# Optimization experiments

Measured on AMD Instinct MI355X. Metric: run time of the kernel, lower is better.

## Reference

```python
import jax, jax.numpy as jnp
import numpy as np

N = 50000      # nodes
E = 800000     # edges (avg degree 16)
IN = 128       # in_dim == hidden_dim*num_heads so residuals fire
D = 32         # hidden_dim (per-head)
H = 4          # num_heads
OUT = 64       # out_dim (final layer has 1 head)
NEG_SLOPE = 0.2
LN_EPS = 1e-5


def setup_inputs() -> dict:
    key = jax.random.key(0)
    ks = jax.random.split(key, 16)
    rn = lambda k, s: jax.random.normal(k, s, jnp.float32) * 0.05
    return {
        "features": jax.random.normal(ks[0], (N, IN), jnp.float32),
        "edge_weight": jax.random.uniform(ks[1], (E,), jnp.float32),
        "src": jax.random.randint(ks[2], (E,), 0, N),
        "dst": jax.random.randint(ks[3], (E,), 0, N),
        "W0": rn(ks[4], (IN, H * D)), "al0": rn(ks[5], (H, D)), "ar0": rn(ks[6], (H, D)), "lam0": jnp.float32(1.0),
        "W1": rn(ks[7], (H * D, H * D)), "al1": rn(ks[8], (H, D)), "ar1": rn(ks[9], (H, D)), "lam1": jnp.float32(1.0),
        "W2": rn(ks[10], (H * D, OUT)), "al2": rn(ks[11], (1, OUT)), "ar2": rn(ks[12], (1, OUT)), "lam2": jnp.float32(1.0),
        "g0": jnp.ones((H * D,), jnp.float32), "b0": jnp.zeros((H * D,), jnp.float32),
        "g1": jnp.ones((H * D,), jnp.float32), "b1": jnp.zeros((H * D,), jnp.float32),
    }


def _gat_layer(h, W, al, ar, lam, src, dst, ew):
    n = h.shape[0]
    heads, d = al.shape
    ft = (h @ W).reshape(n, heads, d)                      # [N,H,D]
    el = jnp.sum(ft * al[None], axis=-1)                   # [N,H]
    er = jnp.sum(ft * ar[None], axis=-1)                   # [N,H]
    e = el[src] + er[dst] + lam * ew[:, None]              # [E,H] u_add_v + weight bias
    e = jax.nn.leaky_relu(e, NEG_SLOPE)
    # edge softmax over incoming edges of each dst node
    m = jax.ops.segment_max(e, dst, num_segments=n)        # [N,H]
    ex = jnp.exp(e - m[dst])
    s = jax.ops.segment_sum(ex, dst, num_segments=n)       # [N,H]
    a = ex / s[dst]                                        # [E,H]
    # u_mul_e + sum aggregation
    msg = ft[src] * a[:, :, None]                          # [E,H,D]
    return jax.ops.segment_sum(msg, dst, num_segments=n)   # [N,H,D]


def _layer_norm(x, g, b):
    mu = jnp.mean(x, axis=-1, keepdims=True)
    var = jnp.mean((x - mu) ** 2, axis=-1, keepdims=True)
    return (x - mu) * jax.lax.rsqrt(var + LN_EPS) * g + b


def _forward(features, edge_weight, src, dst,
             W0, al0, ar0, lam0, W1, al1, ar1, lam1, W2, al2, ar2, lam2,
             g0, b0, g1, b1):
    n = features.shape[0]
    h = features
    # layer 0
    h1 = _gat_layer(h, W0, al0, ar0, lam0, src, dst, edge_weight)
    h1 = jax.nn.elu(h1).reshape(n, -1)
    h1 = _layer_norm(h1, g0, b0)
    if h1.shape == h.shape:
        h1 = h1 + h
    # layer 1
    h2 = _gat_layer(h1, W1, al1, ar1, lam1, src, dst, edge_weight)
    h2 = jax.nn.elu(h2).reshape(n, -1)
    h2 = _layer_norm(h2, g1, b1)
    h2 = h2 + h1
    # layer 2 (single head, no activation)
    out = _gat_layer(h2, W2, al2, ar2, lam2, src, dst, edge_weight).reshape(n, -1)
    return out


def reference(features, edge_weight, src, dst,
              W0, al0, ar0, lam0, W1, al1, ar1, lam1, W2, al2, ar2, lam2,
              g0, b0, g1, b1):
    # eval mode: dropout off and _add_noise is identity, so noisy == clean
    h_clean = _forward(features, edge_weight, src, dst,
                       W0, al0, ar0, lam0, W1, al1, ar1, lam1, W2, al2, ar2, lam2,
                       g0, b0, g1, b1)
    return (h_clean, h_clean)
```

## Files before the change

### kernel.cpp

```cpp
#include <hip/hip_runtime.h>

#define NEG_SLOPE 0.2f
#define LN_EPS 1e-5f

typedef __attribute__((ext_vector_type(8))) short bf16x8;
typedef __attribute__((ext_vector_type(4))) float f32x4;

__device__ inline unsigned short f2bf(float f) {
    unsigned u = __float_as_uint(f);
    unsigned r = u + 0x7FFFu + ((u >> 16) & 1u);
    return (unsigned short)(r >> 16);
}


__global__ void rank_kernel(const int* __restrict__ dst, int* __restrict__ counts,
                            int* __restrict__ rank, int E) {
    int i = blockIdx.x * blockDim.x + threadIdx.x;
    if (i < E) rank[i] = atomicAdd(&counts[dst[i] * 16], 1);
}

__global__ __launch_bounds__(256) void scan1_kernel(const int* __restrict__ counts,
                                                    int* __restrict__ bsum, int n) {
    __shared__ int lds[256];
    int t = threadIdx.x;
    int i = blockIdx.x * 256 + t;
    lds[t] = (i < n) ? counts[i * 16] : 0;
    __syncthreads();
    for (int off = 128; off > 0; off >>= 1) {
        int v = (t < off) ? lds[t + off] : 0;
        __syncthreads();
        if (t < off) lds[t] += v;
        __syncthreads();
    }
    if (t == 0) bsum[blockIdx.x] = lds[0];
}

__global__ __launch_bounds__(256) void scan2_kernel(int* __restrict__ bsum, int nblocks) {
    __shared__ int lds[256];
    int t = threadIdx.x;
    int v0 = (t < nblocks) ? bsum[t] : 0;
    lds[t] = v0;
    __syncthreads();
    for (int off = 1; off < 256; off <<= 1) {
        int v = (t >= off) ? lds[t - off] : 0;
        __syncthreads();
        lds[t] += v;
        __syncthreads();
    }
    if (t < nblocks) bsum[t] = lds[t] - v0;
}

__global__ __launch_bounds__(256) void scan3_kernel(const int* __restrict__ counts,
                                                    const int* __restrict__ bsum,
                                                    int* __restrict__ rowptr, int n, int E) {
    __shared__ int lds[256];
    int t = threadIdx.x;
    int i = blockIdx.x * 256 + t;
    int c = (i < n) ? counts[i * 16] : 0;
    lds[t] = c;
    __syncthreads();
    for (int off = 1; off < 256; off <<= 1) {
        int v = (t >= off) ? lds[t - off] : 0;
        __syncthreads();
        lds[t] += v;
        __syncthreads();
    }
    if (i < n) rowptr[i] = bsum[blockIdx.x] + lds[t] - c;
    if (i == n) rowptr[n] = E;
}

__global__ void place_kernel(const int* __restrict__ src, const int* __restrict__ dst,
                             const float* __restrict__ ew, const int* __restrict__ rowptr,
                             const int* __restrict__ rank, unsigned* __restrict__ edge_p,
                             int E) {
    int i = blockIdx.x * blockDim.x + threadIdx.x;
    if (i < E) {
        int p = rowptr[dst[i]] + rank[i];
        edge_p[p] = ((unsigned)f2bf(ew[i]) << 16) | (unsigned)src[i];
    }
}


__global__ void wcast_kernel(const float* __restrict__ W, unsigned short* __restrict__ Wt,
                             int ncols) {
    int n = blockIdx.x;
    int k = threadIdx.x;
    Wt[n * 128 + k] = f2bf(W[k * ncols + n]);
}


template <int NT, int H>
__global__ __launch_bounds__(256) void gemm_mfma(const float* __restrict__ A,
                                                 const unsigned short* __restrict__ Wt,
                                                 const float* __restrict__ al,
                                                 const float* __restrict__ ar,
                                                 unsigned short* __restrict__ ftb,
                                                 float* __restrict__ el,
                                                 float* __restrict__ er, int n) {
    constexpr int LDA = 136;
    constexpr int D = NT * 16 / H;
    __shared__ unsigned short As[64 * LDA];
    __shared__ unsigned short Ws[NT * 16 * LDA];
    int t = threadIdx.x;
    int row0 = blockIdx.x * 64;

    const float4* A4 = (const float4*)A;
    #pragma unroll
    for (int j = 0; j < 8; ++j) {
        int idx = t + j * 256;
        int r = idx >> 5;
        int c4 = idx & 31;
        int row = row0 + r;
        float4 v = (row < n) ? A4[(size_t)row * 32 + c4] : make_float4(0.f, 0.f, 0.f, 0.f);
        unsigned p0 = (unsigned)f2bf(v.x) | ((unsigned)f2bf(v.y) << 16);
        unsigned p1 = (unsigned)f2bf(v.z) | ((unsigned)f2bf(v.w) << 16);
        *(uint2*)&As[r * LDA + c4 * 4] = make_uint2(p0, p1);
    }
    const uint4* Wg = (const uint4*)Wt;
    #pragma unroll
    for (int j = 0; j < NT; ++j) {
        int idx = t + j * 256;
        int r = idx >> 4;
        int c8 = idx & 15;
        *(uint4*)&Ws[r * LDA + c8 * 8] = Wg[idx];
    }
    __syncthreads();

    int w = t >> 6, lane = t & 63;
    int m = lane & 15, q = lane >> 4;
    f32x4 acc[NT] = {};
    const unsigned short* ap = &As[(w * 16 + m) * LDA + q * 8];
    #pragma unroll
    for (int kk = 0; kk < 4; ++kk) {
        bf16x8 a = *(const bf16x8*)(ap + kk * 32);
        #pragma unroll
        for (int nt = 0; nt < NT; ++nt) {
            bf16x8 b = *(const bf16x8*)&Ws[(nt * 16 + m) * LDA + kk * 32 + q * 8];
            acc[nt] = __builtin_amdgcn_mfma_f32_16x16x32_bf16(a, b, acc[nt], 0, 0, 0);
        }
    }

    float alv[NT], arv[NT];
    #pragma unroll
    for (int nt = 0; nt < NT; ++nt) {
        alv[nt] = al[nt * 16 + m];
        arv[nt] = ar[nt * 16 + m];
    }

    int orow = row0 + w * 16 + q * 4;
    #pragma unroll
    for (int r = 0; r < 4; ++r) {
        int row = orow + r;
        float pl[H] = {}, pr[H] = {};
        #pragma unroll
        for (int nt = 0; nt < NT; ++nt) {
            int h = (nt * 16) / D;
            pl[h] = fmaf(acc[nt][r], alv[nt], pl[h]);
            pr[h] = fmaf(acc[nt][r], arv[nt], pr[h]);
        }
        #pragma unroll
        for (int off = 1; off < 16; off <<= 1) {
            #pragma unroll
            for (int h = 0; h < H; ++h) {
                pl[h] += __shfl_xor(pl[h], off, 64);
                pr[h] += __shfl_xor(pr[h], off, 64);
            }
        }
        if (row < n) {
            #pragma unroll
            for (int nt = 0; nt < NT; ++nt)
                ftb[(size_t)row * (NT * 16) + nt * 16 + m] = f2bf(acc[nt][r]);
            if (m < H) {
                float vl = pl[0], vr = pr[0];
                #pragma unroll
                for (int h = 1; h < H; ++h)
                    if (m == h) { vl = pl[h]; vr = pr[h]; }
                el[row * H + m] = vl;
                er[row * H + m] = vr;
            }
        }
    }
}


__device__ inline void accum8(float* ax, uint4 u, float p) {
    ax[0] = fmaf(p, __uint_as_float(u.x << 16), ax[0]);
    ax[1] = fmaf(p, __uint_as_float(u.x & 0xFFFF0000u), ax[1]);
    ax[2] = fmaf(p, __uint_as_float(u.y << 16), ax[2]);
    ax[3] = fmaf(p, __uint_as_float(u.y & 0xFFFF0000u), ax[3]);
    ax[4] = fmaf(p, __uint_as_float(u.z << 16), ax[4]);
    ax[5] = fmaf(p, __uint_as_float(u.z & 0xFFFF0000u), ax[5]);
    ax[6] = fmaf(p, __uint_as_float(u.w << 16), ax[6]);
    ax[7] = fmaf(p, __uint_as_float(u.w & 0xFFFF0000u), ax[7]);
}

__global__ __launch_bounds__(256) void gat_agg_ln(
    const int* __restrict__ rowptr, const unsigned* __restrict__ edge_p,
    const uint4* __restrict__ ftb4, const float* __restrict__ el,
    const float* __restrict__ er, const float* __restrict__ lam_p,
    const float* __restrict__ g, const float* __restrict__ b,
    const float* __restrict__ prev, float* __restrict__ out, int n) {
    int node = blockIdx.x * 16 + (threadIdx.x >> 4);
    if (node >= n) return;
    int li = threadIdx.x & 15;
    int head = li >> 2;
    float lam = lam_p[0];
    float erv = er[node * 4 + head];
    int s0 = rowptr[node], s1 = rowptr[node + 1];
    float ax[8] = {};
    float s = 0.f;

    int i = s0;
    for (; i + 2 <= s1; i += 2) {
        unsigned e0 = edge_p[i], e1 = edge_p[i + 1];
        unsigned sn0 = e0 & 0xFFFFu, sn1 = e1 & 0xFFFFu;
        uint4 u0 = ftb4[(size_t)sn0 * 16 + li];
        uint4 u1 = ftb4[(size_t)sn1 * 16 + li];
        float l0 = el[sn0 * 4 + head];
        float l1 = el[sn1 * 4 + head];
        float v0 = l0 + erv + lam * __uint_as_float(e0 & 0xFFFF0000u);
        float v1 = l1 + erv + lam * __uint_as_float(e1 & 0xFFFF0000u);
        v0 = fmaxf(v0, NEG_SLOPE * v0);
        v1 = fmaxf(v1, NEG_SLOPE * v1);
        float p0 = __expf(v0), p1 = __expf(v1);
        accum8(ax, u0, p0);
        accum8(ax, u1, p1);
        s += p0 + p1;
    }
    if (i < s1) {
        unsigned e = edge_p[i];
        unsigned sn = e & 0xFFFFu;
        uint4 u = ftb4[(size_t)sn * 16 + li];
        float v = el[sn * 4 + head] + erv + lam * __uint_as_float(e & 0xFFFF0000u);
        v = fmaxf(v, NEG_SLOPE * v);
        float p = __expf(v);
        accum8(ax, u, p);
        s += p;
    }

    float inv = (s > 0.f) ? 1.f / s : 0.f;
    float x[8];
    float sum = 0.f, sq = 0.f;
    #pragma unroll
    for (int d = 0; d < 8; ++d) {
        float v = ax[d] * inv;
        v = (v > 0.f) ? v : expm1f(v);
        x[d] = v;
        sum += v;
        sq += v * v;
    }
    #pragma unroll
    for (int off = 1; off < 16; off <<= 1) {
        sum += __shfl_xor(sum, off, 16);
        sq += __shfl_xor(sq, off, 16);
    }
    float mu = sum * (1.f / 128.f);
    float var = sq * (1.f / 128.f) - mu * mu;
    float rs = rsqrtf(var + LN_EPS);

    const float4* g4 = (const float4*)g;
    const float4* b4 = (const float4*)b;
    const float4* p4 = (const float4*)prev;
    float4* o4 = (float4*)out;
    size_t base = (size_t)node * 32 + li * 2;
    #pragma unroll
    for (int h = 0; h < 2; ++h) {
        float4 gv = g4[li * 2 + h];
        float4 bv = b4[li * 2 + h];
        float4 pv = p4[base + h];
        float4 y;
        y.x = (x[h * 4 + 0] - mu) * rs * gv.x + bv.x + pv.x;
        y.y = (x[h * 4 + 1] - mu) * rs * gv.y + bv.y + pv.y;
        y.z = (x[h * 4 + 2] - mu) * rs * gv.z + bv.z + pv.z;
        y.w = (x[h * 4 + 3] - mu) * rs * gv.w + bv.w + pv.w;
        o4[base + h] = y;
    }
}

__global__ __launch_bounds__(256) void gat_agg_out(
    const int* __restrict__ rowptr, const unsigned* __restrict__ edge_p,
    const uint2* __restrict__ ftb2, const float* __restrict__ el,
    const float* __restrict__ er, const float* __restrict__ lam_p,
    float* __restrict__ out, int n) {
    int node = blockIdx.x * 16 + (threadIdx.x >> 4);
    if (node >= n) return;
    int li = threadIdx.x & 15;
    float lam = lam_p[0];
    float erv = er[node];
    int s0 = rowptr[node], s1 = rowptr[node + 1];
    float ax[4] = {};
    float s = 0.f;

    int i = s0;
    for (; i + 2 <= s1; i += 2) {
        unsigned e0 = edge_p[i], e1 = edge_p[i + 1];
        unsigned sn0 = e0 & 0xFFFFu, sn1 = e1 & 0xFFFFu;
        uint2 u0 = ftb2[(size_t)sn0 * 16 + li];
        uint2 u1 = ftb2[(size_t)sn1 * 16 + li];
        float l0 = el[sn0], l1 = el[sn1];
        float v0 = l0 + erv + lam * __uint_as_float(e0 & 0xFFFF0000u);
        float v1 = l1 + erv + lam * __uint_as_float(e1 & 0xFFFF0000u);
        v0 = fmaxf(v0, NEG_SLOPE * v0);
        v1 = fmaxf(v1, NEG_SLOPE * v1);
        float p0 = __expf(v0), p1 = __expf(v1);
        ax[0] = fmaf(p0, __uint_as_float(u0.x << 16), ax[0]);
        ax[1] = fmaf(p0, __uint_as_float(u0.x & 0xFFFF0000u), ax[1]);
        ax[2] = fmaf(p0, __uint_as_float(u0.y << 16), ax[2]);
        ax[3] = fmaf(p0, __uint_as_float(u0.y & 0xFFFF0000u), ax[3]);
        ax[0] = fmaf(p1, __uint_as_float(u1.x << 16), ax[0]);
        ax[1] = fmaf(p1, __uint_as_float(u1.x & 0xFFFF0000u), ax[1]);
        ax[2] = fmaf(p1, __uint_as_float(u1.y << 16), ax[2]);
        ax[3] = fmaf(p1, __uint_as_float(u1.y & 0xFFFF0000u), ax[3]);
        s += p0 + p1;
    }
    if (i < s1) {
        unsigned e = edge_p[i];
        unsigned sn = e & 0xFFFFu;
        uint2 u = ftb2[(size_t)sn * 16 + li];
        float v = el[sn] + erv + lam * __uint_as_float(e & 0xFFFF0000u);
        v = fmaxf(v, NEG_SLOPE * v);
        float p = __expf(v);
        ax[0] = fmaf(p, __uint_as_float(u.x << 16), ax[0]);
        ax[1] = fmaf(p, __uint_as_float(u.x & 0xFFFF0000u), ax[1]);
        ax[2] = fmaf(p, __uint_as_float(u.y << 16), ax[2]);
        ax[3] = fmaf(p, __uint_as_float(u.y & 0xFFFF0000u), ax[3]);
        s += p;
    }

    float inv = (s > 0.f) ? 1.f / s : 0.f;
    float4 y;
    y.x = ax[0] * inv;
    y.y = ax[1] * inv;
    y.z = ax[2] * inv;
    y.w = ax[3] * inv;
    ((float4*)out)[(size_t)node * 16 + li] = y;
    ((float4*)out)[(size_t)(n + node) * 16 + li] = y;
}


extern "C" void kernel_launch(void* const* d_in, const int* in_sizes, int n_in,
                              void* d_out, int out_size, void* d_ws, size_t ws_size,
                              hipStream_t stream) {
    const float* features = (const float*)d_in[0];
    const float* edge_weight = (const float*)d_in[1];
    const int* src = (const int*)d_in[2];
    const int* dst = (const int*)d_in[3];
    const float* W0 = (const float*)d_in[4];
    const float* al0 = (const float*)d_in[5];
    const float* ar0 = (const float*)d_in[6];
    const float* lam0 = (const float*)d_in[7];
    const float* W1 = (const float*)d_in[8];
    const float* al1 = (const float*)d_in[9];
    const float* ar1 = (const float*)d_in[10];
    const float* lam1 = (const float*)d_in[11];
    const float* W2 = (const float*)d_in[12];
    const float* al2 = (const float*)d_in[13];
    const float* ar2 = (const float*)d_in[14];
    const float* lam2 = (const float*)d_in[15];
    const float* g0 = (const float*)d_in[16];
    const float* b0 = (const float*)d_in[17];
    const float* g1 = (const float*)d_in[18];
    const float* b1 = (const float*)d_in[19];

    const int N = in_sizes[0] / 128;
    const int E = in_sizes[1];

    char* w = (char*)d_ws;
    size_t o = 0;
    auto carve = [&](size_t bytes) {
        char* p = w + o;
        o += (bytes + 255) & ~(size_t)255;
        return p;
    };
    int* counts = (int*)carve((size_t)N * 64);
    int* rowptr = (int*)carve((size_t)(N + 1) * 4);
    int* bsum = (int*)carve(256 * 4);
    int* rank = (int*)carve((size_t)E * 4);
    unsigned* edge_p = (unsigned*)carve((size_t)E * 4);
    unsigned short* ftb = (unsigned short*)carve((size_t)N * 128 * 2);
    float* el = (float*)carve((size_t)N * 4 * 4);
    float* er = (float*)carve((size_t)N * 4 * 4);
    float* h1 = (float*)carve((size_t)N * 128 * 4);
    float* h2 = (float*)carve((size_t)N * 128 * 4);
    unsigned short* Wt0 = (unsigned short*)carve(128 * 128 * 2);
    unsigned short* Wt1 = (unsigned short*)carve(128 * 128 * 2);
    unsigned short* Wt2 = (unsigned short*)carve(64 * 128 * 2);

    const int nscan = (N + 255) / 256;
    const int ngemm = (N + 63) / 64;
    const int nagg = (N + 15) / 16;

    hipMemsetAsync(counts, 0, (size_t)N * 64, stream);
    rank_kernel<<<(E + 255) / 256, 256, 0, stream>>>(dst, counts, rank, E);
    scan1_kernel<<<nscan, 256, 0, stream>>>(counts, bsum, N);
    scan2_kernel<<<1, 256, 0, stream>>>(bsum, nscan);
    scan3_kernel<<<(N + 1 + 255) / 256, 256, 0, stream>>>(counts, bsum, rowptr, N, E);
    place_kernel<<<(E + 255) / 256, 256, 0, stream>>>(src, dst, edge_weight, rowptr,
                                                      rank, edge_p, E);
    wcast_kernel<<<128, 128, 0, stream>>>(W0, Wt0, 128);
    wcast_kernel<<<128, 128, 0, stream>>>(W1, Wt1, 128);
    wcast_kernel<<<64, 128, 0, stream>>>(W2, Wt2, 64);

    gemm_mfma<8, 4><<<ngemm, 256, 0, stream>>>(features, Wt0, al0, ar0, ftb, el, er, N);
    gat_agg_ln<<<nagg, 256, 0, stream>>>(rowptr, edge_p, (const uint4*)ftb,
                                         el, er, lam0, g0, b0, features, h1, N);
    gemm_mfma<8, 4><<<ngemm, 256, 0, stream>>>(h1, Wt1, al1, ar1, ftb, el, er, N);
    gat_agg_ln<<<nagg, 256, 0, stream>>>(rowptr, edge_p, (const uint4*)ftb,
                                         el, er, lam1, g1, b1, h1, h2, N);
    gemm_mfma<4, 1><<<ngemm, 256, 0, stream>>>(h2, Wt2, al2, ar2, ftb, el, er, N);
    gat_agg_out<<<nagg, 256, 0, stream>>>(rowptr, edge_p, (const uint2*)ftb,
                                          el, er, lam2, (float*)d_out, N);
}
```

Baseline: 317.4 us.

## Store hidden activations in bf16 and unroll edge loops by four

Intermediate activations h1/h2 and the input features are now kept in bf16 rather than fp32. A separate cast kernel converts the features, the GEMM loads bf16 rows directly, and the LN/aggregation kernel reads the bf16 residual and writes bf16 output. The three weight-cast launches are merged into one, and the edge aggregation loops are unrolled from two to four edges for more memory-level parallelism. This halves activation traffic, but the residual path now carries bf16 rounding, which lowers accuracy and adds one extra pass over the features.

```diff
diff --git a/kernel.cpp b/kernel.cpp
--- a/kernel.cpp
+++ b/kernel.cpp
@@ -10,6 +10,17 @@
     unsigned u = __float_as_uint(f);
     unsigned r = u + 0x7FFFu + ((u >> 16) & 1u);
     return (unsigned short)(r >> 16);
+}
+
+__device__ inline void unpack8(uint4 u, float* f) {
+    f[0] = __uint_as_float(u.x << 16);
+    f[1] = __uint_as_float(u.x & 0xFFFF0000u);
+    f[2] = __uint_as_float(u.y << 16);
+    f[3] = __uint_as_float(u.y & 0xFFFF0000u);
+    f[4] = __uint_as_float(u.z << 16);
+    f[5] = __uint_as_float(u.z & 0xFFFF0000u);
+    f[6] = __uint_as_float(u.w << 16);
+    f[7] = __uint_as_float(u.w & 0xFFFF0000u);
 }
 
 
@@ -81,16 +92,33 @@
 }
 
 
-__global__ void wcast_kernel(const float* __restrict__ W, unsigned short* __restrict__ Wt,
-                             int ncols) {
-    int n = blockIdx.x;
-    int k = threadIdx.x;
-    Wt[n * 128 + k] = f2bf(W[k * ncols + n]);
+__global__ void fcast_kernel(const float4* __restrict__ in, uint2* __restrict__ out, int n4) {
+    int i = blockIdx.x * blockDim.x + threadIdx.x;
+    if (i < n4) {
+        float4 v = in[i];
+        out[i] = make_uint2((unsigned)f2bf(v.x) | ((unsigned)f2bf(v.y) << 16),
+                            (unsigned)f2bf(v.z) | ((unsigned)f2bf(v.w) << 16));
+    }
+}
+
+__global__ void wcast_all(const float* __restrict__ W0, const float* __restrict__ W1,
+                          const float* __restrict__ W2, unsigned short* __restrict__ Wt0,
+                          unsigned short* __restrict__ Wt1, unsigned short* __restrict__ Wt2) {
+    int bn = blockIdx.x, k = threadIdx.x;
+    if (bn < 128) {
+        Wt0[bn * 128 + k] = f2bf(W0[k * 128 + bn]);
+    } else if (bn < 256) {
+        int c = bn - 128;
+        Wt1[c * 128 + k] = f2bf(W1[k * 128 + c]);
+    } else {
+        int c = bn - 256;
+        Wt2[c * 128 + k] = f2bf(W2[k * 64 + c]);
+    }
 }
 
 
 template <int NT, int H>
-__global__ __launch_bounds__(256) void gemm_mfma(const float* __restrict__ A,
+__global__ __launch_bounds__(256) void gemm_mfma(const uint4* __restrict__ A,
                                                  const unsigned short* __restrict__ Wt,
                                                  const float* __restrict__ al,
                                                  const float* __restrict__ ar,
@@ -104,17 +132,14 @@
     int t = threadIdx.x;
     int row0 = blockIdx.x * 64;
 
-    const float4* A4 = (const float4*)A;
-    #pragma unroll
-    for (int j = 0; j < 8; ++j) {
+    #pragma unroll
+    for (int j = 0; j < 4; ++j) {
         int idx = t + j * 256;
-        int r = idx >> 5;
-        int c4 = idx & 31;
+        int r = idx >> 4;
+        int c8 = idx & 15;
         int row = row0 + r;
-        float4 v = (row < n) ? A4[(size_t)row * 32 + c4] : make_float4(0.f, 0.f, 0.f, 0.f);
-        unsigned p0 = (unsigned)f2bf(v.x) | ((unsigned)f2bf(v.y) << 16);
-        unsigned p1 = (unsigned)f2bf(v.z) | ((unsigned)f2bf(v.w) << 16);
-        *(uint2*)&As[r * LDA + c4 * 4] = make_uint2(p0, p1);
+        uint4 v = (row < n) ? A[(size_t)row * 16 + c8] : make_uint4(0, 0, 0, 0);
+        *(uint4*)&As[r * LDA + c8 * 8] = v;
     }
     const uint4* Wg = (const uint4*)Wt;
     #pragma unroll
@@ -199,7 +224,7 @@
     const uint4* __restrict__ ftb4, const float* __restrict__ el,
     const float* __restrict__ er, const float* __restrict__ lam_p,
     const float* __restrict__ g, const float* __restrict__ b,
-    const float* __restrict__ prev, float* __restrict__ out, int n) {
+    const uint4* __restrict__ prevb, uint4* __restrict__ outb, int n) {
     int node = blockIdx.x * 16 + (threadIdx.x >> 4);
     if (node >= n) return;
     int li = threadIdx.x & 15;
@@ -211,23 +236,33 @@
     float s = 0.f;
 
     int i = s0;
-    for (; i + 2 <= s1; i += 2) {
-        unsigned e0 = edge_p[i], e1 = edge_p[i + 1];
-        unsigned sn0 = e0 & 0xFFFFu, sn1 = e1 & 0xFFFFu;
+    for (; i + 4 <= s1; i += 4) {
+        unsigned e0 = edge_p[i], e1 = edge_p[i + 1], e2 = edge_p[i + 2], e3 = edge_p[i + 3];
+        unsigned sn0 = e0 & 0xFFFFu, sn1 = e1 & 0xFFFFu, sn2 = e2 & 0xFFFFu, sn3 = e3 & 0xFFFFu;
         uint4 u0 = ftb4[(size_t)sn0 * 16 + li];
         uint4 u1 = ftb4[(size_t)sn1 * 16 + li];
+        uint4 u2 = ftb4[(size_t)sn2 * 16 + li];
+        uint4 u3 = ftb4[(size_t)sn3 * 16 + li];
         float l0 = el[sn0 * 4 + head];
         float l1 = el[sn1 * 4 + head];
+        float l2 = el[sn2 * 4 + head];
+        float l3 = el[sn3 * 4 + head];
         float v0 = l0 + erv + lam * __uint_as_float(e0 & 0xFFFF0000u);
         float v1 = l1 + erv + lam * __uint_as_float(e1 & 0xFFFF0000u);
+        float v2 = l2 + erv + lam * __uint_as_float(e2 & 0xFFFF0000u);
+        float v3 = l3 + erv + lam * __uint_as_float(e3 & 0xFFFF0000u);
         v0 = fmaxf(v0, NEG_SLOPE * v0);
         v1 = fmaxf(v1, NEG_SLOPE * v1);
-        float p0 = __expf(v0), p1 = __expf(v1);
+        v2 = fmaxf(v2, NEG_SLOPE * v2);
+        v3 = fmaxf(v3, NEG_SLOPE * v3);
+        float p0 = __expf(v0), p1 = __expf(v1), p2 = __expf(v2), p3 = __expf(v3);
         accum8(ax, u0, p0);
         accum8(ax, u1, p1);
-        s += p0 + p1;
-    }
-    if (i < s1) {
+        accum8(ax, u2, p2);
+        accum8(ax, u3, p3);
+        s += (p0 + p1) + (p2 + p3);
+    }
+    for (; i < s1; ++i) {
         unsigned e = edge_p[i];
         unsigned sn = e & 0xFFFFu;
         uint4 u = ftb4[(size_t)sn * 16 + li];
@@ -260,21 +295,24 @@
 
     const float4* g4 = (const float4*)g;
     const float4* b4 = (const float4*)b;
-    const float4* p4 = (const float4*)prev;
-    float4* o4 = (float4*)out;
-    size_t base = (size_t)node * 32 + li * 2;
+    float pv[8];
+    unpack8(prevb[(size_t)node * 16 + li], pv);
+    float y[8];
     #pragma unroll
     for (int h = 0; h < 2; ++h) {
         float4 gv = g4[li * 2 + h];
         float4 bv = b4[li * 2 + h];
-        float4 pv = p4[base + h];
-        float4 y;
-        y.x = (x[h * 4 + 0] - mu) * rs * gv.x + bv.x + pv.x;
-        y.y = (x[h * 4 + 1] - mu) * rs * gv.y + bv.y + pv.y;
-        y.z = (x[h * 4 + 2] - mu) * rs * gv.z + bv.z + pv.z;
-        y.w = (x[h * 4 + 3] - mu) * rs * gv.w + bv.w + pv.w;
-        o4[base + h] = y;
-    }
+        y[h * 4 + 0] = (x[h * 4 + 0] - mu) * rs * gv.x + bv.x + pv[h * 4 + 0];
+        y[h * 4 + 1] = (x[h * 4 + 1] - mu) * rs * gv.y + bv.y + pv[h * 4 + 1];
+        y[h * 4 + 2] = (x[h * 4 + 2] - mu) * rs * gv.z + bv.z + pv[h * 4 + 2];
+        y[h * 4 + 3] = (x[h * 4 + 3] - mu) * rs * gv.w + bv.w + pv[h * 4 + 3];
+    }
+    uint4 o;
+    o.x = (unsigned)f2bf(y[0]) | ((unsigned)f2bf(y[1]) << 16);
+    o.y = (unsigned)f2bf(y[2]) | ((unsigned)f2bf(y[3]) << 16);
+    o.z = (unsigned)f2bf(y[4]) | ((unsigned)f2bf(y[5]) << 16);
+    o.w = (unsigned)f2bf(y[6]) | ((unsigned)f2bf(y[7]) << 16);
+    outb[(size_t)node * 16 + li] = o;
 }
 
 __global__ __launch_bounds__(256) void gat_agg_out(
@@ -292,17 +330,23 @@
     float s = 0.f;
 
     int i = s0;
-    for (; i + 2 <= s1; i += 2) {
-        unsigned e0 = edge_p[i], e1 = edge_p[i + 1];
-        unsigned sn0 = e0 & 0xFFFFu, sn1 = e1 & 0xFFFFu;
+    for (; i + 4 <= s1; i += 4) {
+        unsigned e0 = edge_p[i], e1 = edge_p[i + 1], e2 = edge_p[i + 2], e3 = edge_p[i + 3];
+        unsigned sn0 = e0 & 0xFFFFu, sn1 = e1 & 0xFFFFu, sn2 = e2 & 0xFFFFu, sn3 = e3 & 0xFFFFu;
         uint2 u0 = ftb2[(size_t)sn0 * 16 + li];
         uint2 u1 = ftb2[(size_t)sn1 * 16 + li];
-        float l0 = el[sn0], l1 = el[sn1];
+        uint2 u2 = ftb2[(size_t)sn2 * 16 + li];
+        uint2 u3 = ftb2[(size_t)sn3 * 16 + li];
+        float l0 = el[sn0], l1 = el[sn1], l2 = el[sn2], l3 = el[sn3];
         float v0 = l0 + erv + lam * __uint_as_float(e0 & 0xFFFF0000u);
         float v1 = l1 + erv + lam * __uint_as_float(e1 & 0xFFFF0000u);
+        float v2 = l2 + erv + lam * __uint_as_float(e2 & 0xFFFF0000u);
+        float v3 = l3 + erv + lam * __uint_as_float(e3 & 0xFFFF0000u);
         v0 = fmaxf(v0, NEG_SLOPE * v0);
         v1 = fmaxf(v1, NEG_SLOPE * v1);
-        float p0 = __expf(v0), p1 = __expf(v1);
+        v2 = fmaxf(v2, NEG_SLOPE * v2);
+        v3 = fmaxf(v3, NEG_SLOPE * v3);
+        float p0 = __expf(v0), p1 = __expf(v1), p2 = __expf(v2), p3 = __expf(v3);
         ax[0] = fmaf(p0, __uint_as_float(u0.x << 16), ax[0]);
         ax[1] = fmaf(p0, __uint_as_float(u0.x & 0xFFFF0000u), ax[1]);
         ax[2] = fmaf(p0, __uint_as_float(u0.y << 16), ax[2]);
@@ -311,9 +355,17 @@
         ax[1] = fmaf(p1, __uint_as_float(u1.x & 0xFFFF0000u), ax[1]);
         ax[2] = fmaf(p1, __uint_as_float(u1.y << 16), ax[2]);
         ax[3] = fmaf(p1, __uint_as_float(u1.y & 0xFFFF0000u), ax[3]);
-        s += p0 + p1;
-    }
-    if (i < s1) {
+        ax[0] = fmaf(p2, __uint_as_float(u2.x << 16), ax[0]);
+        ax[1] = fmaf(p2, __uint_as_float(u2.x & 0xFFFF0000u), ax[1]);
+        ax[2] = fmaf(p2, __uint_as_float(u2.y << 16), ax[2]);
+        ax[3] = fmaf(p2, __uint_as_float(u2.y & 0xFFFF0000u), ax[3]);
+        ax[0] = fmaf(p3, __uint_as_float(u3.x << 16), ax[0]);
+        ax[1] = fmaf(p3, __uint_as_float(u3.x & 0xFFFF0000u), ax[1]);
+        ax[2] = fmaf(p3, __uint_as_float(u3.y << 16), ax[2]);
+        ax[3] = fmaf(p3, __uint_as_float(u3.y & 0xFFFF0000u), ax[3]);
+        s += (p0 + p1) + (p2 + p3);
+    }
+    for (; i < s1; ++i) {
         unsigned e = edge_p[i];
         unsigned sn = e & 0xFFFFu;
         uint2 u = ftb2[(size_t)sn * 16 + li];
@@ -378,10 +430,11 @@
     int* rank = (int*)carve((size_t)E * 4);
     unsigned* edge_p = (unsigned*)carve((size_t)E * 4);
     unsigned short* ftb = (unsigned short*)carve((size_t)N * 128 * 2);
+    unsigned short* f0b = (unsigned short*)carve((size_t)N * 128 * 2);
+    unsigned short* h1 = (unsigned short*)carve((size_t)N * 128 * 2);
+    unsigned short* h2 = (unsigned short*)carve((size_t)N * 128 * 2);
     float* el = (float*)carve((size_t)N * 4 * 4);
     float* er = (float*)carve((size_t)N * 4 * 4);
-    float* h1 = (float*)carve((size_t)N * 128 * 4);
-    float* h2 = (float*)carve((size_t)N * 128 * 4);
     unsigned short* Wt0 = (unsigned short*)carve(128 * 128 * 2);
     unsigned short* Wt1 = (unsigned short*)carve(128 * 128 * 2);
     unsigned short* Wt2 = (unsigned short*)carve(64 * 128 * 2);
@@ -397,17 +450,20 @@
     scan3_kernel<<<(N + 1 + 255) / 256, 256, 0, stream>>>(counts, bsum, rowptr, N, E);
     place_kernel<<<(E + 255) / 256, 256, 0, stream>>>(src, dst, edge_weight, rowptr,
                                                       rank, edge_p, E);
-    wcast_kernel<<<128, 128, 0, stream>>>(W0, Wt0, 128);
-    wcast_kernel<<<128, 128, 0, stream>>>(W1, Wt1, 128);
-    wcast_kernel<<<64, 128, 0, stream>>>(W2, Wt2, 64);
-
-    gemm_mfma<8, 4><<<ngemm, 256, 0, stream>>>(features, Wt0, al0, ar0, ftb, el, er, N);
-    gat_agg_ln<<<nagg, 256, 0, stream>>>(rowptr, edge_p, (const uint4*)ftb,
-                                         el, er, lam0, g0, b0, features, h1, N);
-    gemm_mfma<8, 4><<<ngemm, 256, 0, stream>>>(h1, Wt1, al1, ar1, ftb, el, er, N);
-    gat_agg_ln<<<nagg, 256, 0, stream>>>(rowptr, edge_p, (const uint4*)ftb,
-                                         el, er, lam1, g1, b1, h1, h2, N);
-    gemm_mfma<4, 1><<<ngemm, 256, 0, stream>>>(h2, Wt2, al2, ar2, ftb, el, er, N);
+    fcast_kernel<<<(N * 32 + 255) / 256, 256, 0, stream>>>((const float4*)features,
+                                                           (uint2*)f0b, N * 32);
+    wcast_all<<<320, 128, 0, stream>>>(W0, W1, W2, Wt0, Wt1, Wt2);
+
+    gemm_mfma<8, 4><<<ngemm, 256, 0, stream>>>((const uint4*)f0b, Wt0, al0, ar0,
+                                               ftb, el, er, N);
+    gat_agg_ln<<<nagg, 256, 0, stream>>>(rowptr, edge_p, (const uint4*)ftb, el, er, lam0,
+                                         g0, b0, (const uint4*)f0b, (uint4*)h1, N);
+    gemm_mfma<8, 4><<<ngemm, 256, 0, stream>>>((const uint4*)h1, Wt1, al1, ar1,
+                                               ftb, el, er, N);
+    gat_agg_ln<<<nagg, 256, 0, stream>>>(rowptr, edge_p, (const uint4*)ftb, el, er, lam1,
+                                         g1, b1, (const uint4*)h1, (uint4*)h2, N);
+    gemm_mfma<4, 1><<<ngemm, 256, 0, stream>>>((const uint4*)h2, Wt2, al2, ar2,
+                                               ftb, el, er, N);
     gat_agg_out<<<nagg, 256, 0, stream>>>(rowptr, edge_p, (const uint2*)ftb,
                                           el, er, lam2, (float*)d_out, N);
 }
```

Result: faster. 307.9 us (-3.0%).
